# Kernel tuning notes

Hardware: AMD Instinct MI355X
Metric: run time of the kernel (lower is better)

The kernel has to match this reference:

```python
import jax, jax.numpy as jnp
import numpy as np
from jax import lax

H = 128


def _ema_scan(x):
    # x: [B, T, N, F] -> EMA along T: s_t = 0.9*s_{t-1} + 0.1*x_t
    xt = jnp.moveaxis(x, 1, 0)  # [T, B, N, F]

    def step(s, xi):
        s = s * 0.9 + xi * 0.1
        return s, s

    _, ys = lax.scan(step, jnp.zeros_like(xt[0]), xt)
    return jnp.moveaxis(ys, 0, 1)  # [B, T, N, F]


def setup_inputs() -> dict:
    key = jax.random.key(0)
    k1, k2, k3, k4, k5 = jax.random.split(key, 5)
    B, T, N = 4, 96, 512
    x = jax.random.normal(k1, (B, T, N, H), dtype=jnp.float32)
    s = 1.0 / np.sqrt(H)
    W_exp = jax.random.uniform(k2, (2 * H, H), jnp.float32, -s, s)
    b_exp = jax.random.uniform(k3, (2 * H,), jnp.float32, -s, s)
    W_con = jax.random.uniform(k4, (H, H), jnp.float32, -s, s)
    b_con = jax.random.uniform(k5, (H,), jnp.float32, -s, s)
    return {"spatial_temporal_representation": x, "W_exp": W_exp, "b_exp": b_exp,
            "W_con": W_con, "b_con": b_con}


def reference(spatial_temporal_representation, W_exp, b_exp, W_con, b_con):
    x = spatial_temporal_representation  # [B,T,N,H]
    expanded = jnp.einsum('btnh,oh->btno', x, W_exp) + b_exp  # [B,T,N,2H]
    state_primary, state_gating = jnp.split(expanded, 2, axis=-1)
    gated_activation = jax.nn.sigmoid(_ema_scan(state_gating))
    out = jnp.einsum('btnh,oh->btno', state_primary * gated_activation, W_con) + b_con
    return out
```

## Files before the change

kernel.cpp:

```cpp
#include <hip/hip_runtime.h>

#define B_DIM 4
#define T_DIM 96
#define N_DIM 512
#define H_DIM 128
#define NH    (N_DIM * H_DIM)

#define WS_WEXP  0
#define WS_WCON  32768
#define WS_L     49152
#define WS_TOTAL 58368

typedef __attribute__((ext_vector_type(8))) short short8;
typedef __attribute__((ext_vector_type(4))) float f32x4;

__device__ __forceinline__ unsigned short f2b_rh(float f) {
    union { float f; unsigned u; } c; c.f = f;
    return (unsigned short)((c.u + 0x8000u) >> 16);
}
__device__ __forceinline__ unsigned pack_bf16_2(float a, float b) {
    union { float f; unsigned u; } ca, cb; ca.f = a; cb.f = b;
    return __builtin_amdgcn_perm(cb.u + 0x8000u, ca.u + 0x8000u, 0x07060302u);
}
__device__ __forceinline__ float b2f(unsigned short s) {
    union { unsigned u; float f; } c; c.u = ((unsigned)s) << 16;
    return c.f;
}

extern "C" __global__ void prep_kernel(const float* __restrict__ Wexp,
                                       const float* __restrict__ Wcon,
                                       unsigned short* __restrict__ ws) {
    int i = blockIdx.x * 256 + threadIdx.x;
    if (i < 32768) {
        ws[WS_WEXP + i] = f2b_rh(Wexp[i]);
    } else if (i < 49152) {
        int j = i - 32768;
        ws[WS_WCON + j] = f2b_rh(Wcon[j]);
    } else if (i < WS_TOTAL) {
        int j = i - 49152;
        int t = j / 96, k = j - t * 96;
        float v = 0.0f;
        if (k <= t) v = 0.1f * __expf((float)(t - k) * -0.1053605157f);
        ws[WS_L + j] = f2b_rh(v);
    }
}

extern "C" __global__ __launch_bounds__(256, 3)
void mamba_fused(const float* __restrict__ x,
                 const unsigned short* __restrict__ ws,
                 const float* __restrict__ b_exp,
                 const float* __restrict__ b_con,
                 float* __restrict__ out)
{
    __shared__ __align__(16) unsigned short prim[T_DIM * 136];
    __shared__ __align__(16) unsigned short gpg[H_DIM * 104];

    const int tid  = threadIdx.x;
    const int wave = tid >> 6;
    const int lane = tid & 63;
    const int q    = lane >> 4;
    const int l16  = lane & 15;

    const int blk = blockIdx.x;
    const int n   = blk & (N_DIM - 1);
    const int b   = blk >> 9;

    const float* xg = x + ((size_t)b * T_DIM * N_DIM + (size_t)n) * H_DIM;

    short8 wf[4][4];
    float4 bias1[4];
    {
        const int obase = wave * 64;
        const unsigned short* wsW = ws + WS_WEXP;
        for (int ot = 0; ot < 4; ++ot) {
            const unsigned short* wrow = wsW + (size_t)(obase + ot * 16 + l16) * H_DIM + q * 8;
            for (int k0 = 0; k0 < 4; ++k0)
                wf[ot][k0] = *(const short8*)(wrow + k0 * 32);
            bias1[ot] = *(const float4*)(b_exp + obase + ot * 16 + q * 4);
        }
    }

    for (int mt = 0; mt < 6; ++mt) {
        const float* xrow = xg + (size_t)(mt * 16 + l16) * NH + q * 8;
        short8 bfr[4];
        for (int k0 = 0; k0 < 4; ++k0) {
            float4 v0 = *(const float4*)(xrow + k0 * 32);
            float4 v1 = *(const float4*)(xrow + k0 * 32 + 4);
            union { unsigned u[4]; short8 s; } p;
            p.u[0] = pack_bf16_2(v0.x, v0.y);
            p.u[1] = pack_bf16_2(v0.z, v0.w);
            p.u[2] = pack_bf16_2(v1.x, v1.y);
            p.u[3] = pack_bf16_2(v1.z, v1.w);
            bfr[k0] = p.s;
        }
        const int tcol = mt * 16 + l16;
        for (int ot = 0; ot < 4; ++ot) {
            f32x4 acc = {0.f, 0.f, 0.f, 0.f};
            for (int k0 = 0; k0 < 4; ++k0)
                acc = __builtin_amdgcn_mfma_f32_16x16x32_bf16(wf[ot][k0], bfr[k0], acc, 0, 0, 0);
            const int o = wave * 64 + ot * 16 + q * 4;
            float r0 = acc[0] + bias1[ot].x, r1 = acc[1] + bias1[ot].y;
            float r2 = acc[2] + bias1[ot].z, r3 = acc[3] + bias1[ot].w;
            if (wave < 2) {
                union { unsigned u[2]; ushort4 s; } pk;
                pk.u[0] = pack_bf16_2(r0, r1);
                pk.u[1] = pack_bf16_2(r2, r3);
                *(ushort4*)&prim[tcol * 136 + o] = pk.s;
            } else {
                const int g = o - 128;
                gpg[(g + 0) * 104 + tcol] = f2b_rh(r0);
                gpg[(g + 1) * 104 + tcol] = f2b_rh(r1);
                gpg[(g + 2) * 104 + tcol] = f2b_rh(r2);
                gpg[(g + 3) * 104 + tcol] = f2b_rh(r3);
            }
        }
    }
    __syncthreads();

    f32x4 eacc[2][6];
    for (int ht = 0; ht < 2; ++ht)
        for (int tt = 0; tt < 6; ++tt)
            eacc[ht][tt] = (f32x4){0.f, 0.f, 0.f, 0.f};
    {
        const unsigned short* wsL = ws + WS_L;
        for (int kf = 0; kf < 3; ++kf) {
            short8 af[2];
            for (int ht = 0; ht < 2; ++ht) {
                const int h = (wave * 2 + ht) * 16 + l16;
                af[ht] = *(const short8*)&gpg[h * 104 + kf * 32 + q * 8];
            }
            for (int tt = 0; tt < 6; ++tt) {
                short8 bf = *(const short8*)(wsL + (size_t)(tt * 16 + l16) * 96 + kf * 32 + q * 8);
                eacc[0][tt] = __builtin_amdgcn_mfma_f32_16x16x32_bf16(af[0], bf, eacc[0][tt], 0, 0, 0);
                eacc[1][tt] = __builtin_amdgcn_mfma_f32_16x16x32_bf16(af[1], bf, eacc[1][tt], 0, 0, 0);
            }
        }
    }

    short8 wc[2][4];
    float4 bias2[2];
    {
        const int obase = wave * 32;
        const unsigned short* wsW = ws + WS_WCON;
        for (int ot = 0; ot < 2; ++ot) {
            const unsigned short* wrow = wsW + (size_t)(obase + ot * 16 + l16) * H_DIM + q * 8;
            for (int k0 = 0; k0 < 4; ++k0)
                wc[ot][k0] = *(const short8*)(wrow + k0 * 32);
            bias2[ot] = *(const float4*)(b_con + obase + ot * 16 + q * 4);
        }
    }
    __syncthreads();

    for (int ht = 0; ht < 2; ++ht) {
        const int hb = (wave * 2 + ht) * 16 + q * 4;
        for (int tt = 0; tt < 6; ++tt) {
            const int t = tt * 16 + l16;
            ushort4 pv = *(const ushort4*)&prim[t * 136 + hb];
            f32x4 s = eacc[ht][tt];
            float sg0 = __fdividef(1.f, 1.f + __expf(-s[0]));
            float sg1 = __fdividef(1.f, 1.f + __expf(-s[1]));
            float sg2 = __fdividef(1.f, 1.f + __expf(-s[2]));
            float sg3 = __fdividef(1.f, 1.f + __expf(-s[3]));
            float p0 = b2f(pv.x) * sg0, p1 = b2f(pv.y) * sg1;
            float p2 = b2f(pv.z) * sg2, p3 = b2f(pv.w) * sg3;
            union { unsigned u[2]; ushort4 s; } pk;
            pk.u[0] = pack_bf16_2(p0, p1);
            pk.u[1] = pack_bf16_2(p2, p3);
            *(ushort4*)&gpg[t * 136 + hb] = pk.s;
        }
    }
    __syncthreads();

    float* og = out + ((size_t)b * T_DIM * N_DIM + (size_t)n) * H_DIM;
    for (int mt = 0; mt < 6; ++mt) {
        short8 bfr[4];
        const unsigned short* prow = &gpg[(mt * 16 + l16) * 136];
        for (int k0 = 0; k0 < 4; ++k0)
            bfr[k0] = *(const short8*)(prow + k0 * 32 + q * 8);
        const int t = mt * 16 + l16;
        for (int ot = 0; ot < 2; ++ot) {
            f32x4 acc = {0.f, 0.f, 0.f, 0.f};
            for (int k0 = 0; k0 < 4; ++k0)
                acc = __builtin_amdgcn_mfma_f32_16x16x32_bf16(wc[ot][k0], bfr[k0], acc, 0, 0, 0);
            const int o = wave * 32 + ot * 16 + q * 4;
            float4 v;
            v.x = acc[0] + bias2[ot].x;
            v.y = acc[1] + bias2[ot].y;
            v.z = acc[2] + bias2[ot].z;
            v.w = acc[3] + bias2[ot].w;
            *(float4*)(og + (size_t)t * NH + o) = v;
        }
    }
}

extern "C" void kernel_launch(void* const* d_in, const int* in_sizes, int n_in,
                              void* d_out, int out_size, void* d_ws, size_t ws_size,
                              hipStream_t stream) {
    const float* x     = (const float*)d_in[0];
    const float* W_exp = (const float*)d_in[1];
    const float* b_exp = (const float*)d_in[2];
    const float* W_con = (const float*)d_in[3];
    const float* b_con = (const float*)d_in[4];
    float* out = (float*)d_out;
    unsigned short* ws = (unsigned short*)d_ws;

    hipLaunchKernelGGL(prep_kernel, dim3(WS_TOTAL / 256), dim3(256), 0, stream,
                       W_exp, W_con, ws);
    hipLaunchKernelGGL(mamba_fused, dim3(B_DIM * N_DIM), dim3(256), 0, stream,
                       x, ws, b_exp, b_con, out);
}
```

Before: 230.6 us.

## Use 8 waves per block with each wave owning matching primary and gate channels

Doubles the block to 512 threads so each wave computes 16 primary and the matching 16 gate channels. The primary result stays in registers, which removes the prim shared buffer and two block-wide barriers; only a wave-local LDS wait remains before the scan matmul. The expand bias is applied after the EMA as a closed-form geometric factor instead of being added before. Every wave still reads all 128 x channels per time row, so x is now loaded redundantly by eight waves instead of four, and register pressure under launch_bounds(512,6) may cause spills.

Result: slower. 293.1 us (+27.1%).

```diff
diff --git a/kernel.cpp b/kernel.cpp
--- a/kernel.cpp
+++ b/kernel.cpp
@@ -22,8 +22,8 @@
     union { float f; unsigned u; } ca, cb; ca.f = a; cb.f = b;
     return __builtin_amdgcn_perm(cb.u + 0x8000u, ca.u + 0x8000u, 0x07060302u);
 }
-__device__ __forceinline__ float b2f(unsigned short s) {
-    union { unsigned u; float f; } c; c.u = ((unsigned)s) << 16;
+__device__ __forceinline__ float u2f(unsigned u) {
+    union { unsigned u; float f; } c; c.u = u;
     return c.f;
 }
 
@@ -45,15 +45,15 @@
     }
 }
 
-extern "C" __global__ __launch_bounds__(256, 3)
+extern "C" __global__ __launch_bounds__(512, 6)
 void mamba_fused(const float* __restrict__ x,
                  const unsigned short* __restrict__ ws,
                  const float* __restrict__ b_exp,
                  const float* __restrict__ b_con,
                  float* __restrict__ out)
 {
-    __shared__ __align__(16) unsigned short prim[T_DIM * 136];
-    __shared__ __align__(16) unsigned short gpg[H_DIM * 104];
+    __shared__ __align__(16) unsigned short gateT[H_DIM * 104];
+    __shared__ __align__(16) unsigned short pg[T_DIM * 136];
 
     const int tid  = threadIdx.x;
     const int wave = tid >> 6;
@@ -67,18 +67,17 @@
 
     const float* xg = x + ((size_t)b * T_DIM * N_DIM + (size_t)n) * H_DIM;
 
-    short8 wf[4][4];
-    float4 bias1[4];
+    short8 wp[4], wg[4];
     {
-        const int obase = wave * 64;
-        const unsigned short* wsW = ws + WS_WEXP;
-        for (int ot = 0; ot < 4; ++ot) {
-            const unsigned short* wrow = wsW + (size_t)(obase + ot * 16 + l16) * H_DIM + q * 8;
-            for (int k0 = 0; k0 < 4; ++k0)
-                wf[ot][k0] = *(const short8*)(wrow + k0 * 32);
-            bias1[ot] = *(const float4*)(b_exp + obase + ot * 16 + q * 4);
+        const unsigned short* wrp = ws + WS_WEXP + (size_t)(wave * 16 + l16) * H_DIM + q * 8;
+        const unsigned short* wrg = wrp + 128 * H_DIM;
+        for (int k0 = 0; k0 < 4; ++k0) {
+            wp[k0] = *(const short8*)(wrp + k0 * 32);
+            wg[k0] = *(const short8*)(wrg + k0 * 32);
         }
     }
+
+    unsigned pacc[6][2];
 
     for (int mt = 0; mt < 6; ++mt) {
         const float* xrow = xg + (size_t)(mt * 16 + l16) * NH + q * 8;
@@ -93,103 +92,84 @@
             p.u[3] = pack_bf16_2(v1.z, v1.w);
             bfr[k0] = p.s;
         }
-        const int tcol = mt * 16 + l16;
-        for (int ot = 0; ot < 4; ++ot) {
-            f32x4 acc = {0.f, 0.f, 0.f, 0.f};
-            for (int k0 = 0; k0 < 4; ++k0)
-                acc = __builtin_amdgcn_mfma_f32_16x16x32_bf16(wf[ot][k0], bfr[k0], acc, 0, 0, 0);
-            const int o = wave * 64 + ot * 16 + q * 4;
-            float r0 = acc[0] + bias1[ot].x, r1 = acc[1] + bias1[ot].y;
-            float r2 = acc[2] + bias1[ot].z, r3 = acc[3] + bias1[ot].w;
-            if (wave < 2) {
-                union { unsigned u[2]; ushort4 s; } pk;
-                pk.u[0] = pack_bf16_2(r0, r1);
-                pk.u[1] = pack_bf16_2(r2, r3);
-                *(ushort4*)&prim[tcol * 136 + o] = pk.s;
-            } else {
-                const int g = o - 128;
-                gpg[(g + 0) * 104 + tcol] = f2b_rh(r0);
-                gpg[(g + 1) * 104 + tcol] = f2b_rh(r1);
-                gpg[(g + 2) * 104 + tcol] = f2b_rh(r2);
-                gpg[(g + 3) * 104 + tcol] = f2b_rh(r3);
-            }
+        f32x4 ap = {0.f, 0.f, 0.f, 0.f};
+        f32x4 ag = {0.f, 0.f, 0.f, 0.f};
+        for (int k0 = 0; k0 < 4; ++k0) {
+            ap = __builtin_amdgcn_mfma_f32_16x16x32_bf16(wp[k0], bfr[k0], ap, 0, 0, 0);
+            ag = __builtin_amdgcn_mfma_f32_16x16x32_bf16(wg[k0], bfr[k0], ag, 0, 0, 0);
         }
+        pacc[mt][0] = pack_bf16_2(ap[0], ap[1]);
+        pacc[mt][1] = pack_bf16_2(ap[2], ap[3]);
+        unsigned short* gr = &gateT[(wave * 16 + q * 4) * 104 + mt * 16 + l16];
+        gr[0]       = f2b_rh(ag[0]);
+        gr[104]     = f2b_rh(ag[1]);
+        gr[2 * 104] = f2b_rh(ag[2]);
+        gr[3 * 104] = f2b_rh(ag[3]);
     }
-    __syncthreads();
 
-    f32x4 eacc[2][6];
-    for (int ht = 0; ht < 2; ++ht)
-        for (int tt = 0; tt < 6; ++tt)
-            eacc[ht][tt] = (f32x4){0.f, 0.f, 0.f, 0.f};
+    asm volatile("s_waitcnt lgkmcnt(0)" ::: "memory");
+    __builtin_amdgcn_sched_barrier(0);
+
+    f32x4 eacc[6];
+    for (int tt = 0; tt < 6; ++tt) eacc[tt] = (f32x4){0.f, 0.f, 0.f, 0.f};
     {
         const unsigned short* wsL = ws + WS_L;
         for (int kf = 0; kf < 3; ++kf) {
-            short8 af[2];
-            for (int ht = 0; ht < 2; ++ht) {
-                const int h = (wave * 2 + ht) * 16 + l16;
-                af[ht] = *(const short8*)&gpg[h * 104 + kf * 32 + q * 8];
-            }
+            short8 af = *(const short8*)&gateT[(wave * 16 + l16) * 104 + kf * 32 + q * 8];
             for (int tt = 0; tt < 6; ++tt) {
                 short8 bf = *(const short8*)(wsL + (size_t)(tt * 16 + l16) * 96 + kf * 32 + q * 8);
-                eacc[0][tt] = __builtin_amdgcn_mfma_f32_16x16x32_bf16(af[0], bf, eacc[0][tt], 0, 0, 0);
-                eacc[1][tt] = __builtin_amdgcn_mfma_f32_16x16x32_bf16(af[1], bf, eacc[1][tt], 0, 0, 0);
+                eacc[tt] = __builtin_amdgcn_mfma_f32_16x16x32_bf16(af, bf, eacc[tt], 0, 0, 0);
             }
         }
     }
 
-    short8 wc[2][4];
-    float4 bias2[2];
+    short8 wc[4];
+    float4 bias2, bp, bg;
     {
-        const int obase = wave * 32;
-        const unsigned short* wsW = ws + WS_WCON;
-        for (int ot = 0; ot < 2; ++ot) {
-            const unsigned short* wrow = wsW + (size_t)(obase + ot * 16 + l16) * H_DIM + q * 8;
-            for (int k0 = 0; k0 < 4; ++k0)
-                wc[ot][k0] = *(const short8*)(wrow + k0 * 32);
-            bias2[ot] = *(const float4*)(b_con + obase + ot * 16 + q * 4);
-        }
+        const unsigned short* wrc = ws + WS_WCON + (size_t)(wave * 16 + l16) * H_DIM + q * 8;
+        for (int k0 = 0; k0 < 4; ++k0)
+            wc[k0] = *(const short8*)(wrc + k0 * 32);
+        bias2 = *(const float4*)(b_con + wave * 16 + q * 4);
+        bp    = *(const float4*)(b_exp + wave * 16 + q * 4);
+        bg    = *(const float4*)(b_exp + 128 + wave * 16 + q * 4);
     }
-    __syncthreads();
 
-    for (int ht = 0; ht < 2; ++ht) {
-        const int hb = (wave * 2 + ht) * 16 + q * 4;
-        for (int tt = 0; tt < 6; ++tt) {
-            const int t = tt * 16 + l16;
-            ushort4 pv = *(const ushort4*)&prim[t * 136 + hb];
-            f32x4 s = eacc[ht][tt];
-            float sg0 = __fdividef(1.f, 1.f + __expf(-s[0]));
-            float sg1 = __fdividef(1.f, 1.f + __expf(-s[1]));
-            float sg2 = __fdividef(1.f, 1.f + __expf(-s[2]));
-            float sg3 = __fdividef(1.f, 1.f + __expf(-s[3]));
-            float p0 = b2f(pv.x) * sg0, p1 = b2f(pv.y) * sg1;
-            float p2 = b2f(pv.z) * sg2, p3 = b2f(pv.w) * sg3;
-            union { unsigned u[2]; ushort4 s; } pk;
-            pk.u[0] = pack_bf16_2(p0, p1);
-            pk.u[1] = pack_bf16_2(p2, p3);
-            *(ushort4*)&gpg[t * 136 + hb] = pk.s;
-        }
+    for (int tt = 0; tt < 6; ++tt) {
+        const int t = tt * 16 + l16;
+        const float c = 1.0f - __expf((float)(t + 1) * -0.1053605157f);
+        f32x4 s = eacc[tt];
+        float sg0 = __fdividef(1.f, 1.f + __expf(-(s[0] + bg.x * c)));
+        float sg1 = __fdividef(1.f, 1.f + __expf(-(s[1] + bg.y * c)));
+        float sg2 = __fdividef(1.f, 1.f + __expf(-(s[2] + bg.z * c)));
+        float sg3 = __fdividef(1.f, 1.f + __expf(-(s[3] + bg.w * c)));
+        unsigned u0 = pacc[tt][0], u1 = pacc[tt][1];
+        float p0 = (u2f(u0 << 16)          + bp.x) * sg0;
+        float p1 = (u2f(u0 & 0xffff0000u)  + bp.y) * sg1;
+        float p2 = (u2f(u1 << 16)          + bp.z) * sg2;
+        float p3 = (u2f(u1 & 0xffff0000u)  + bp.w) * sg3;
+        union { unsigned u[2]; ushort4 s; } pk;
+        pk.u[0] = pack_bf16_2(p0, p1);
+        pk.u[1] = pack_bf16_2(p2, p3);
+        *(ushort4*)&pg[t * 136 + wave * 16 + q * 4] = pk.s;
     }
     __syncthreads();
 
     float* og = out + ((size_t)b * T_DIM * N_DIM + (size_t)n) * H_DIM;
     for (int mt = 0; mt < 6; ++mt) {
         short8 bfr[4];
-        const unsigned short* prow = &gpg[(mt * 16 + l16) * 136];
+        const unsigned short* prow = &pg[(mt * 16 + l16) * 136];
         for (int k0 = 0; k0 < 4; ++k0)
             bfr[k0] = *(const short8*)(prow + k0 * 32 + q * 8);
+        f32x4 acc = {0.f, 0.f, 0.f, 0.f};
+        for (int k0 = 0; k0 < 4; ++k0)
+            acc = __builtin_amdgcn_mfma_f32_16x16x32_bf16(wc[k0], bfr[k0], acc, 0, 0, 0);
         const int t = mt * 16 + l16;
-        for (int ot = 0; ot < 2; ++ot) {
-            f32x4 acc = {0.f, 0.f, 0.f, 0.f};
-            for (int k0 = 0; k0 < 4; ++k0)
-                acc = __builtin_amdgcn_mfma_f32_16x16x32_bf16(wc[ot][k0], bfr[k0], acc, 0, 0, 0);
-            const int o = wave * 32 + ot * 16 + q * 4;
-            float4 v;
-            v.x = acc[0] + bias2[ot].x;
-            v.y = acc[1] + bias2[ot].y;
-            v.z = acc[2] + bias2[ot].z;
-            v.w = acc[3] + bias2[ot].w;
-            *(float4*)(og + (size_t)t * NH + o) = v;
-        }
+        float4 v;
+        v.x = acc[0] + bias2.x;
+        v.y = acc[1] + bias2.y;
+        v.z = acc[2] + bias2.z;
+        v.w = acc[3] + bias2.w;
+        *(float4*)(og + (size_t)t * NH + wave * 16 + q * 4) = v;
     }
 }
 
@@ -206,6 +186,6 @@
 
     hipLaunchKernelGGL(prep_kernel, dim3(WS_TOTAL / 256), dim3(256), 0, stream,
                        W_exp, W_con, ws);
-    hipLaunchKernelGGL(mamba_fused, dim3(B_DIM * N_DIM), dim3(256), 0, stream,
+    hipLaunchKernelGGL(mamba_fused, dim3(B_DIM * N_DIM), dim3(512), 0, stream,
                        x, ws, b_exp, b_con, out);
 }
```

## Stage x in LDS, keep primary in registers, skip zero EMA tiles

Applied to the files above, without the earlier changes.

The x tile is loaded with coalesced float4 reads, converted to bf16, and staged once in shared memory instead of each wave reading strided rows from global memory. Each wave now computes matching primary and gate channels, so the primary result stays packed in registers instead of round-tripping through a shared buffer. The expand bias is folded analytically into the EMA as b*(1-0.9^(t+1)). MFMAs on the upper-triangular zero blocks of the EMA matrix are skipped. The cost is more register pressure under the 3-blocks-per-SM launch bound, plus a hand-placed waitcnt and sched barrier.

Result: faster. 224.7 us (-2.5%).

```diff
diff --git a/kernel.cpp b/kernel.cpp
--- a/kernel.cpp
+++ b/kernel.cpp
@@ -22,8 +22,8 @@
     union { float f; unsigned u; } ca, cb; ca.f = a; cb.f = b;
     return __builtin_amdgcn_perm(cb.u + 0x8000u, ca.u + 0x8000u, 0x07060302u);
 }
-__device__ __forceinline__ float b2f(unsigned short s) {
-    union { unsigned u; float f; } c; c.u = ((unsigned)s) << 16;
+__device__ __forceinline__ float u2f(unsigned u) {
+    union { unsigned u; float f; } c; c.u = u;
     return c.f;
 }
 
@@ -52,8 +52,8 @@
                  const float* __restrict__ b_con,
                  float* __restrict__ out)
 {
-    __shared__ __align__(16) unsigned short prim[T_DIM * 136];
-    __shared__ __align__(16) unsigned short gpg[H_DIM * 104];
+    __shared__ __align__(16) unsigned short gateT[H_DIM * 104];
+    __shared__ __align__(16) unsigned short xpg[T_DIM * 136];
 
     const int tid  = threadIdx.x;
     const int wave = tid >> 6;
@@ -67,122 +67,147 @@
 
     const float* xg = x + ((size_t)b * T_DIM * N_DIM + (size_t)n) * H_DIM;
 
-    short8 wf[4][4];
-    float4 bias1[4];
     {
-        const int obase = wave * 64;
-        const unsigned short* wsW = ws + WS_WEXP;
-        for (int ot = 0; ot < 4; ++ot) {
-            const unsigned short* wrow = wsW + (size_t)(obase + ot * 16 + l16) * H_DIM + q * 8;
-            for (int k0 = 0; k0 < 4; ++k0)
-                wf[ot][k0] = *(const short8*)(wrow + k0 * 32);
-            bias1[ot] = *(const float4*)(b_exp + obase + ot * 16 + q * 4);
-        }
-    }
-
+        const int r2    = lane >> 5;
+        const int c     = lane & 31;
+        const int rbase = wave * 2 + r2;
+        #pragma unroll
+        for (int i = 0; i < 12; ++i) {
+            const int r = i * 8 + rbase;
+            float4 v = *(const float4*)(xg + (size_t)r * NH + c * 4);
+            union { unsigned u[2]; ushort4 s; } pk;
+            pk.u[0] = pack_bf16_2(v.x, v.y);
+            pk.u[1] = pack_bf16_2(v.z, v.w);
+            *(ushort4*)&xpg[r * 136 + c * 4] = pk.s;
+        }
+    }
+
+    short8 wp[2][4], wg[2][4];
+    #pragma unroll
+    for (int ot = 0; ot < 2; ++ot) {
+        const unsigned short* wrp = ws + WS_WEXP + (size_t)((wave * 2 + ot) * 16 + l16) * H_DIM + q * 8;
+        #pragma unroll
+        for (int k0 = 0; k0 < 4; ++k0) {
+            wp[ot][k0] = *(const short8*)(wrp + k0 * 32);
+            wg[ot][k0] = *(const short8*)(wrp + 128 * H_DIM + k0 * 32);
+        }
+    }
+    __syncthreads();
+
+    unsigned pacc[2][6][2];
+
+    #pragma unroll
     for (int mt = 0; mt < 6; ++mt) {
-        const float* xrow = xg + (size_t)(mt * 16 + l16) * NH + q * 8;
         short8 bfr[4];
+        #pragma unroll
+        for (int k0 = 0; k0 < 4; ++k0)
+            bfr[k0] = *(const short8*)&xpg[(mt * 16 + l16) * 136 + k0 * 32 + q * 8];
+        f32x4 ap0 = {0.f,0.f,0.f,0.f}, ap1 = {0.f,0.f,0.f,0.f};
+        f32x4 ag0 = {0.f,0.f,0.f,0.f}, ag1 = {0.f,0.f,0.f,0.f};
+        #pragma unroll
         for (int k0 = 0; k0 < 4; ++k0) {
-            float4 v0 = *(const float4*)(xrow + k0 * 32);
-            float4 v1 = *(const float4*)(xrow + k0 * 32 + 4);
-            union { unsigned u[4]; short8 s; } p;
-            p.u[0] = pack_bf16_2(v0.x, v0.y);
-            p.u[1] = pack_bf16_2(v0.z, v0.w);
-            p.u[2] = pack_bf16_2(v1.x, v1.y);
-            p.u[3] = pack_bf16_2(v1.z, v1.w);
-            bfr[k0] = p.s;
-        }
-        const int tcol = mt * 16 + l16;
-        for (int ot = 0; ot < 4; ++ot) {
-            f32x4 acc = {0.f, 0.f, 0.f, 0.f};
-            for (int k0 = 0; k0 < 4; ++k0)
-                acc = __builtin_amdgcn_mfma_f32_16x16x32_bf16(wf[ot][k0], bfr[k0], acc, 0, 0, 0);
-            const int o = wave * 64 + ot * 16 + q * 4;
-            float r0 = acc[0] + bias1[ot].x, r1 = acc[1] + bias1[ot].y;
-            float r2 = acc[2] + bias1[ot].z, r3 = acc[3] + bias1[ot].w;
-            if (wave < 2) {
-                union { unsigned u[2]; ushort4 s; } pk;
-                pk.u[0] = pack_bf16_2(r0, r1);
-                pk.u[1] = pack_bf16_2(r2, r3);
-                *(ushort4*)&prim[tcol * 136 + o] = pk.s;
-            } else {
-                const int g = o - 128;
-                gpg[(g + 0) * 104 + tcol] = f2b_rh(r0);
-                gpg[(g + 1) * 104 + tcol] = f2b_rh(r1);
-                gpg[(g + 2) * 104 + tcol] = f2b_rh(r2);
-                gpg[(g + 3) * 104 + tcol] = f2b_rh(r3);
-            }
-        }
-    }
-    __syncthreads();
+            ap0 = __builtin_amdgcn_mfma_f32_16x16x32_bf16(wp[0][k0], bfr[k0], ap0, 0, 0, 0);
+            ap1 = __builtin_amdgcn_mfma_f32_16x16x32_bf16(wp[1][k0], bfr[k0], ap1, 0, 0, 0);
+            ag0 = __builtin_amdgcn_mfma_f32_16x16x32_bf16(wg[0][k0], bfr[k0], ag0, 0, 0, 0);
+            ag1 = __builtin_amdgcn_mfma_f32_16x16x32_bf16(wg[1][k0], bfr[k0], ag1, 0, 0, 0);
+        }
+        pacc[0][mt][0] = pack_bf16_2(ap0[0], ap0[1]);
+        pacc[0][mt][1] = pack_bf16_2(ap0[2], ap0[3]);
+        pacc[1][mt][0] = pack_bf16_2(ap1[0], ap1[1]);
+        pacc[1][mt][1] = pack_bf16_2(ap1[2], ap1[3]);
+        unsigned short* gr0 = &gateT[((wave * 2 + 0) * 16 + q * 4) * 104 + mt * 16 + l16];
+        gr0[0]       = f2b_rh(ag0[0]);
+        gr0[104]     = f2b_rh(ag0[1]);
+        gr0[2 * 104] = f2b_rh(ag0[2]);
+        gr0[3 * 104] = f2b_rh(ag0[3]);
+        unsigned short* gr1 = &gateT[((wave * 2 + 1) * 16 + q * 4) * 104 + mt * 16 + l16];
+        gr1[0]       = f2b_rh(ag1[0]);
+        gr1[104]     = f2b_rh(ag1[1]);
+        gr1[2 * 104] = f2b_rh(ag1[2]);
+        gr1[3 * 104] = f2b_rh(ag1[3]);
+    }
+
+    asm volatile("s_waitcnt lgkmcnt(0)" ::: "memory");
+    __builtin_amdgcn_sched_barrier(0);
 
     f32x4 eacc[2][6];
+    #pragma unroll
     for (int ht = 0; ht < 2; ++ht)
+        #pragma unroll
         for (int tt = 0; tt < 6; ++tt)
             eacc[ht][tt] = (f32x4){0.f, 0.f, 0.f, 0.f};
     {
         const unsigned short* wsL = ws + WS_L;
+        #pragma unroll
         for (int kf = 0; kf < 3; ++kf) {
-            short8 af[2];
-            for (int ht = 0; ht < 2; ++ht) {
-                const int h = (wave * 2 + ht) * 16 + l16;
-                af[ht] = *(const short8*)&gpg[h * 104 + kf * 32 + q * 8];
+            short8 af0 = *(const short8*)&gateT[((wave * 2 + 0) * 16 + l16) * 104 + kf * 32 + q * 8];
+            short8 af1 = *(const short8*)&gateT[((wave * 2 + 1) * 16 + l16) * 104 + kf * 32 + q * 8];
+            #pragma unroll
+            for (int tt = 0; tt < 6; ++tt) {
+                if (tt < 2 * kf) continue;
+                short8 bf = *(const short8*)(wsL + (size_t)(tt * 16 + l16) * 96 + kf * 32 + q * 8);
+                eacc[0][tt] = __builtin_amdgcn_mfma_f32_16x16x32_bf16(af0, bf, eacc[0][tt], 0, 0, 0);
+                eacc[1][tt] = __builtin_amdgcn_mfma_f32_16x16x32_bf16(af1, bf, eacc[1][tt], 0, 0, 0);
             }
-            for (int tt = 0; tt < 6; ++tt) {
-                short8 bf = *(const short8*)(wsL + (size_t)(tt * 16 + l16) * 96 + kf * 32 + q * 8);
-                eacc[0][tt] = __builtin_amdgcn_mfma_f32_16x16x32_bf16(af[0], bf, eacc[0][tt], 0, 0, 0);
-                eacc[1][tt] = __builtin_amdgcn_mfma_f32_16x16x32_bf16(af[1], bf, eacc[1][tt], 0, 0, 0);
-            }
         }
     }
 
     short8 wc[2][4];
-    float4 bias2[2];
-    {
-        const int obase = wave * 32;
-        const unsigned short* wsW = ws + WS_WCON;
-        for (int ot = 0; ot < 2; ++ot) {
-            const unsigned short* wrow = wsW + (size_t)(obase + ot * 16 + l16) * H_DIM + q * 8;
-            for (int k0 = 0; k0 < 4; ++k0)
-                wc[ot][k0] = *(const short8*)(wrow + k0 * 32);
-            bias2[ot] = *(const float4*)(b_con + obase + ot * 16 + q * 4);
-        }
+    float4 bias2[2], bp[2], bgv[2];
+    #pragma unroll
+    for (int ot = 0; ot < 2; ++ot) {
+        const int o = (wave * 2 + ot) * 16;
+        const unsigned short* wrc = ws + WS_WCON + (size_t)(o + l16) * H_DIM + q * 8;
+        #pragma unroll
+        for (int k0 = 0; k0 < 4; ++k0)
+            wc[ot][k0] = *(const short8*)(wrc + k0 * 32);
+        bias2[ot] = *(const float4*)(b_con + o + q * 4);
+        bp[ot]    = *(const float4*)(b_exp + o + q * 4);
+        bgv[ot]   = *(const float4*)(b_exp + 128 + o + q * 4);
     }
     __syncthreads();
 
-    for (int ht = 0; ht < 2; ++ht) {
-        const int hb = (wave * 2 + ht) * 16 + q * 4;
+    #pragma unroll
+    for (int ot = 0; ot < 2; ++ot) {
+        const int hb = (wave * 2 + ot) * 16 + q * 4;
+        #pragma unroll
         for (int tt = 0; tt < 6; ++tt) {
             const int t = tt * 16 + l16;
-            ushort4 pv = *(const ushort4*)&prim[t * 136 + hb];
-            f32x4 s = eacc[ht][tt];
-            float sg0 = __fdividef(1.f, 1.f + __expf(-s[0]));
-            float sg1 = __fdividef(1.f, 1.f + __expf(-s[1]));
-            float sg2 = __fdividef(1.f, 1.f + __expf(-s[2]));
-            float sg3 = __fdividef(1.f, 1.f + __expf(-s[3]));
-            float p0 = b2f(pv.x) * sg0, p1 = b2f(pv.y) * sg1;
-            float p2 = b2f(pv.z) * sg2, p3 = b2f(pv.w) * sg3;
+            const float c = 1.0f - __expf((float)(t + 1) * -0.1053605157f);
+            f32x4 s = eacc[ot][tt];
+            float sg0 = __fdividef(1.f, 1.f + __expf(-(s[0] + bgv[ot].x * c)));
+            float sg1 = __fdividef(1.f, 1.f + __expf(-(s[1] + bgv[ot].y * c)));
+            float sg2 = __fdividef(1.f, 1.f + __expf(-(s[2] + bgv[ot].z * c)));
+            float sg3 = __fdividef(1.f, 1.f + __expf(-(s[3] + bgv[ot].w * c)));
+            unsigned u0 = pacc[ot][tt][0], u1 = pacc[ot][tt][1];
+            float p0 = (u2f(u0 << 16)         + bp[ot].x) * sg0;
+            float p1 = (u2f(u0 & 0xffff0000u) + bp[ot].y) * sg1;
+            float p2 = (u2f(u1 << 16)         + bp[ot].z) * sg2;
+            float p3 = (u2f(u1 & 0xffff0000u) + bp[ot].w) * sg3;
             union { unsigned u[2]; ushort4 s; } pk;
             pk.u[0] = pack_bf16_2(p0, p1);
             pk.u[1] = pack_bf16_2(p2, p3);
-            *(ushort4*)&gpg[t * 136 + hb] = pk.s;
+            *(ushort4*)&xpg[t * 136 + hb] = pk.s;
         }
     }
     __syncthreads();
 
     float* og = out + ((size_t)b * T_DIM * N_DIM + (size_t)n) * H_DIM;
+    #pragma unroll
     for (int mt = 0; mt < 6; ++mt) {
         short8 bfr[4];
-        const unsigned short* prow = &gpg[(mt * 16 + l16) * 136];
+        const unsigned short* prow = &xpg[(mt * 16 + l16) * 136];
+        #pragma unroll
         for (int k0 = 0; k0 < 4; ++k0)
             bfr[k0] = *(const short8*)(prow + k0 * 32 + q * 8);
         const int t = mt * 16 + l16;
+        #pragma unroll
         for (int ot = 0; ot < 2; ++ot) {
             f32x4 acc = {0.f, 0.f, 0.f, 0.f};
+            #pragma unroll
             for (int k0 = 0; k0 < 4; ++k0)
                 acc = __builtin_amdgcn_mfma_f32_16x16x32_bf16(wc[ot][k0], bfr[k0], acc, 0, 0, 0);
-            const int o = wave * 32 + ot * 16 + q * 4;
+            const int o = (wave * 2 + ot) * 16 + q * 4;
             float4 v;
             v.x = acc[0] + bias2[ot].x;
             v.y = acc[1] + bias2[ot].y;
```
